# Kernel tuning notes

Hardware: AMD Instinct MI355X
Metric: run time of the kernel (lower is better)

The kernel has to match this reference:

```python
import jax, jax.numpy as jnp
import numpy as np


def _normalized_histograms(x, num_bins):
    # x: (B, C, H, W) in [0, 1]. Returns (B*C, num_bins) normalized histograms.
    B, C, H, W = x.shape
    rows = B * C
    flat = x.reshape(rows, H * W)
    # torch.histc semantics on [0,1]: bin i covers [i/nb, (i+1)/nb), last bin
    # also includes 1.0 -> floor(x*nb) clipped to [0, nb-1].
    idx = jnp.clip(jnp.floor(flat * num_bins).astype(jnp.int32), 0, num_bins - 1)
    # Offset each (b,c) row into its own segment range, one segment_sum for all.
    seg = (idx + jnp.arange(rows, dtype=jnp.int32)[:, None] * num_bins).reshape(-1)
    counts = jax.ops.segment_sum(
        jnp.ones(seg.shape, dtype=x.dtype), seg, num_segments=rows * num_bins
    ).reshape(rows, num_bins)
    return counts / counts.sum(axis=1, keepdims=True)


def setup_inputs() -> dict:
    key = jax.random.key(0)
    k1, k2 = jax.random.split(key)
    B, C, H, W = 16, 3, 1024, 1024
    output = jax.random.uniform(k1, (B, C, H, W), dtype=jnp.float32)
    target = jax.random.uniform(k2, (B, C, H, W), dtype=jnp.float32)
    return {"output": output, "target": target, "num_bins": 256}


def reference(output, target, num_bins):
    h_out = _normalized_histograms(output, num_bins)
    h_tgt = _normalized_histograms(target, num_bins)
    # sum over (b,c) of mean-over-bins L1, divided by B*C == global mean.
    return jnp.abs(h_out - h_tgt).mean()
```

## Files before the change

### kernel.cpp

```cpp
#include <hip/hip_runtime.h>


#define NB       256
#define HW_N     (1024 * 1024)
#define ROWS     48
#define SEGS     (2 * ROWS)
#define SUBS     16
#define THREADS  256
#define NWAVES   (THREADS / 64)


__global__ __launch_bounds__(THREADS) void hist_kernel(
    const float* __restrict__ out_t,
    const float* __restrict__ tgt_t,
    unsigned int* __restrict__ partials)
{
    __shared__ unsigned int lh[NWAVES][NB];
    const int tid = threadIdx.x;
    const int wid = tid >> 6;

    #pragma unroll
    for (int w = 0; w < NWAVES; ++w)
        for (int i = tid; i < NB; i += THREADS) lh[w][i] = 0u;
    __syncthreads();

    const int blk = blockIdx.x;
    const int seg = blk / SUBS;
    const int sub = blk % SUBS;
    const float* src = (seg < ROWS) ? out_t : tgt_t;
    const int row = (seg < ROWS) ? seg : (seg - ROWS);

    const int elems = HW_N / SUBS;
    const size_t base = (size_t)row * HW_N + (size_t)sub * elems;
    const float4* __restrict__ p = reinterpret_cast<const float4*>(src + base);

    unsigned int* __restrict__ h = lh[wid];
    for (int t = 0; t < 16; ++t) {
        const int i0 = t * 1024 + tid;
        float4 a = p[i0];
        float4 b = p[i0 + 256];
        float4 c = p[i0 + 512];
        float4 d = p[i0 + 768];
        #define BIN(x) min(max((int)floorf((x) * (float)NB), 0), NB - 1)
        atomicAdd(&h[BIN(a.x)], 1u); atomicAdd(&h[BIN(a.y)], 1u);
        atomicAdd(&h[BIN(a.z)], 1u); atomicAdd(&h[BIN(a.w)], 1u);
        atomicAdd(&h[BIN(b.x)], 1u); atomicAdd(&h[BIN(b.y)], 1u);
        atomicAdd(&h[BIN(b.z)], 1u); atomicAdd(&h[BIN(b.w)], 1u);
        atomicAdd(&h[BIN(c.x)], 1u); atomicAdd(&h[BIN(c.y)], 1u);
        atomicAdd(&h[BIN(c.z)], 1u); atomicAdd(&h[BIN(c.w)], 1u);
        atomicAdd(&h[BIN(d.x)], 1u); atomicAdd(&h[BIN(d.y)], 1u);
        atomicAdd(&h[BIN(d.z)], 1u); atomicAdd(&h[BIN(d.w)], 1u);
        #undef BIN
    }
    __syncthreads();

    unsigned int* __restrict__ g = partials + (size_t)blk * NB;
    for (int i = tid; i < NB; i += THREADS) {
        unsigned int c = lh[0][i] + lh[1][i] + lh[2][i] + lh[3][i];
        g[i] = c;
    }
}

__global__ __launch_bounds__(THREADS) void rowdiff_kernel(
    const unsigned int* __restrict__ partials,
    unsigned int* __restrict__ gsum)
{
    const int r = blockIdx.x;
    const int bin = threadIdx.x;
    unsigned int a = 0, b = 0;
    #pragma unroll
    for (int s = 0; s < SUBS; ++s) {
        a += partials[((size_t)(r)         * SUBS + s) * NB + bin];
        b += partials[((size_t)(ROWS + r)  * SUBS + s) * NB + bin];
    }
    int d = (int)a - (int)b;
    unsigned int ad = (unsigned int)((d < 0) ? -d : d);

    __shared__ unsigned int s[THREADS];
    s[bin] = ad;
    __syncthreads();
    for (int off = THREADS / 2; off >= 1; off >>= 1) {
        if (bin < off) s[bin] += s[bin + off];
        __syncthreads();
    }
    if (bin == 0) atomicAdd(gsum, s[0]);
}

__global__ void finalize_kernel(const unsigned int* __restrict__ gsum,
                                float* __restrict__ out)
{
    double v = (double)(*gsum) /
               ((double)HW_N * (double)ROWS * (double)NB);
    out[0] = (float)v;
}

extern "C" void kernel_launch(void* const* d_in, const int* in_sizes, int n_in,
                              void* d_out, int out_size, void* d_ws, size_t ws_size,
                              hipStream_t stream) {
    const float* out_t = (const float*)d_in[0];
    const float* tgt_t = (const float*)d_in[1];
    unsigned int* partials = (unsigned int*)d_ws;
    unsigned int* gsum = partials + (size_t)SEGS * SUBS * NB;
    float* out = (float*)d_out;

    hipMemsetAsync(gsum, 0, sizeof(unsigned int), stream);

    hist_kernel<<<dim3(SEGS * SUBS), dim3(THREADS), 0, stream>>>(out_t, tgt_t, partials);
    rowdiff_kernel<<<dim3(ROWS), dim3(THREADS), 0, stream>>>(partials, gsum);
    finalize_kernel<<<1, 1, 0, stream>>>(gsum, out);
}
```

Measured before the change: 395.9 us.

## Interleave 8 sub-histograms per bin in LDS and software-pipeline loads

Replaces the per-wave LDS histograms with 8 interleaved copies per bin, selected by lane index, so lanes in a wave that hit the same bin spread across copies and banks and contend less on LDS atomics. The main loop now issues the next iteration's four float4 loads before doing the current iteration's atomics, overlapping global memory latency with LDS work. The final reduction reads each bin's 8 copies with two uint4 LDS loads. LDS use grows to 8 KB per block and the prefetch needs more registers.

New measurement: 392.6 us. No clear change (-0.8%).

```diff
diff --git a/kernel.cpp b/kernel.cpp
--- a/kernel.cpp
+++ b/kernel.cpp
@@ -7,7 +7,7 @@
 #define SEGS     (2 * ROWS)
 #define SUBS     16
 #define THREADS  256
-#define NWAVES   (THREADS / 64)
+#define NSUB     8
 
 
 __global__ __launch_bounds__(THREADS) void hist_kernel(
@@ -15,50 +15,56 @@
     const float* __restrict__ tgt_t,
     unsigned int* __restrict__ partials)
 {
-    __shared__ unsigned int lh[NWAVES][NB];
+    __shared__ unsigned int lh[NB * NSUB];
     const int tid = threadIdx.x;
-    const int wid = tid >> 6;
+    const int sub_off = tid & (NSUB - 1);
 
     #pragma unroll
-    for (int w = 0; w < NWAVES; ++w)
-        for (int i = tid; i < NB; i += THREADS) lh[w][i] = 0u;
+    for (int i = tid; i < NB * NSUB; i += THREADS) lh[i] = 0u;
     __syncthreads();
 
     const int blk = blockIdx.x;
     const int seg = blk / SUBS;
-    const int sub = blk % SUBS;
+    const int sb  = blk % SUBS;
     const float* src = (seg < ROWS) ? out_t : tgt_t;
     const int row = (seg < ROWS) ? seg : (seg - ROWS);
 
     const int elems = HW_N / SUBS;
-    const size_t base = (size_t)row * HW_N + (size_t)sub * elems;
+    const size_t base = (size_t)row * HW_N + (size_t)sb * elems;
     const float4* __restrict__ p = reinterpret_cast<const float4*>(src + base);
 
-    unsigned int* __restrict__ h = lh[wid];
-    for (int t = 0; t < 16; ++t) {
-        const int i0 = t * 1024 + tid;
-        float4 a = p[i0];
-        float4 b = p[i0 + 256];
-        float4 c = p[i0 + 512];
-        float4 d = p[i0 + 768];
-        #define BIN(x) min(max((int)floorf((x) * (float)NB), 0), NB - 1)
-        atomicAdd(&h[BIN(a.x)], 1u); atomicAdd(&h[BIN(a.y)], 1u);
-        atomicAdd(&h[BIN(a.z)], 1u); atomicAdd(&h[BIN(a.w)], 1u);
-        atomicAdd(&h[BIN(b.x)], 1u); atomicAdd(&h[BIN(b.y)], 1u);
-        atomicAdd(&h[BIN(b.z)], 1u); atomicAdd(&h[BIN(b.w)], 1u);
-        atomicAdd(&h[BIN(c.x)], 1u); atomicAdd(&h[BIN(c.y)], 1u);
-        atomicAdd(&h[BIN(c.z)], 1u); atomicAdd(&h[BIN(c.w)], 1u);
-        atomicAdd(&h[BIN(d.x)], 1u); atomicAdd(&h[BIN(d.y)], 1u);
-        atomicAdd(&h[BIN(d.z)], 1u); atomicAdd(&h[BIN(d.w)], 1u);
-        #undef BIN
+    #define BIN(x) min(max((int)floorf((x) * (float)NB), 0), NB - 1)
+    #define ACC(v) do { \
+        atomicAdd(&lh[(BIN(v.x) << 3) | sub_off], 1u); \
+        atomicAdd(&lh[(BIN(v.y) << 3) | sub_off], 1u); \
+        atomicAdd(&lh[(BIN(v.z) << 3) | sub_off], 1u); \
+        atomicAdd(&lh[(BIN(v.w) << 3) | sub_off], 1u); \
+    } while (0)
+
+    float4 c0 = p[tid];
+    float4 c1 = p[tid + 256];
+    float4 c2 = p[tid + 512];
+    float4 c3 = p[tid + 768];
+    #pragma unroll 1
+    for (int t = 0; t < 15; ++t) {
+        const int i1 = (t + 1) * 1024 + tid;
+        float4 n0 = p[i1];
+        float4 n1 = p[i1 + 256];
+        float4 n2 = p[i1 + 512];
+        float4 n3 = p[i1 + 768];
+        ACC(c0); ACC(c1); ACC(c2); ACC(c3);
+        c0 = n0; c1 = n1; c2 = n2; c3 = n3;
     }
+    ACC(c0); ACC(c1); ACC(c2); ACC(c3);
+    #undef ACC
+    #undef BIN
     __syncthreads();
 
-    unsigned int* __restrict__ g = partials + (size_t)blk * NB;
-    for (int i = tid; i < NB; i += THREADS) {
-        unsigned int c = lh[0][i] + lh[1][i] + lh[2][i] + lh[3][i];
-        g[i] = c;
-    }
+    const uint4* lh4 = reinterpret_cast<const uint4*>(lh);
+    uint4 a = lh4[tid * 2];
+    uint4 b = lh4[tid * 2 + 1];
+    unsigned int c = a.x + a.y + a.z + a.w + b.x + b.y + b.z + b.w;
+    partials[(size_t)blk * NB + tid] = c;
 }
 
 __global__ __launch_bounds__(THREADS) void rowdiff_kernel(
@@ -70,8 +76,8 @@
     unsigned int a = 0, b = 0;
     #pragma unroll
     for (int s = 0; s < SUBS; ++s) {
-        a += partials[((size_t)(r)         * SUBS + s) * NB + bin];
-        b += partials[((size_t)(ROWS + r)  * SUBS + s) * NB + bin];
+        a += partials[((size_t)(r)        * SUBS + s) * NB + bin];
+        b += partials[((size_t)(ROWS + r) * SUBS + s) * NB + bin];
     }
     int d = (int)a - (int)b;
     unsigned int ad = (unsigned int)((d < 0) ? -d : d);
```
